# Performance work log

Measured on AMD Instinct MI355X. Metric: run time of the kernel, lower is better.

## Reference

```python
import math
import jax, jax.numpy as jnp
import numpy as np

RCR = 5.2   # radial cutoff
RCA = 3.5   # angular cutoff
B, N, T, KR, KA = 256, 24, 4, 16, 32

# static index tables (depend only on N)
_NIDX = np.array([[j for j in range(N) if j != i] for i in range(N)])  # [N, N-1] neighbors excluding self
_I1, _I2 = np.triu_indices(N - 1, k=1)                                  # pair combinations, P = C(N-1,2)


def setup_inputs() -> dict:
    key = jax.random.key(0)
    k1, k2 = jax.random.split(key)
    coords = jax.random.normal(k1, (B, N, 3), dtype=jnp.float32)
    atom_types = jax.random.randint(k2, (N,), 0, T)
    EtaR = jnp.full((T, KR), 16.0, dtype=jnp.float32)
    ShfR = jnp.tile(jnp.linspace(0.9, 4.95, KR, dtype=jnp.float32), (T, 1))
    Zeta = jnp.full((T, KA), 32.0, dtype=jnp.float32)
    ShfZ = jnp.tile(jnp.tile(jnp.linspace(0.9, 3.525, 8, dtype=jnp.float32), 4), (T, 1))
    EtaA = jnp.full((T, KA), 8.0, dtype=jnp.float32)
    ShfA = jnp.tile(jnp.repeat(jnp.linspace(0.3927, 2.7489, 4, dtype=jnp.float32), 8), (T, 1))
    return dict(coords=coords, atom_types=atom_types, EtaR=EtaR, ShfR=ShfR,
                Zeta=Zeta, ShfZ=ShfZ, EtaA=EtaA, ShfA=ShfA)


def reference(coords, atom_types, EtaR, ShfR, Zeta, ShfZ, EtaA, ShfA):
    # pairwise vectors excluding self: rij[b,i,k] = coords[b,i] - coords[b, j_k], j_k != i
    rij = coords[:, :, None, :] - coords[:, _NIDX, :]                      # [B,N,N-1,3]

    # gather per-atom parameter rows: [N, K] -> broadcast as [1,N,1,K]
    etaR = EtaR[atom_types][None, :, None, :]
    shfR = ShfR[atom_types][None, :, None, :]
    zeta = Zeta[atom_types][None, :, None, :]
    shfZ = ShfZ[atom_types][None, :, None, :]
    etaA = EtaA[atom_types][None, :, None, :]
    shfA = ShfA[atom_types][None, :, None, :]

    # ---- radial G2 ----
    dij = jnp.linalg.norm(rij, axis=3)                                     # [B,N,N-1]
    fij = 0.5 * (jnp.cos(dij * (math.pi / RCR)) + 1.0)
    g2 = jnp.sum(jnp.exp(-etaR * (dij[..., None] - shfR) ** 2) * fij[..., None], axis=2)  # [B,N,KR]

    # ---- angular G3 (ANI) ----
    r12 = rij[:, :, _I1]                                                   # [B,N,P,3]
    r13 = rij[:, :, _I2]
    d12 = jnp.linalg.norm(r12, axis=3)                                     # [B,N,P]
    d13 = jnp.linalg.norm(r13, axis=3)
    f12 = 0.5 * (jnp.cos(d12 * (math.pi / RCA)) + 1.0)
    f13 = 0.5 * (jnp.cos(d13 * (math.pi / RCA)) + 1.0)
    cosine = jnp.einsum('bnpc,bnpc->bnp', r12, r13) / (d12 * d13)
    cosine = jnp.clip(cosine, -1.0 + 1e-7, 1.0 - 1e-7)  # numerical guard for acos
    cosang = jnp.cos(jnp.arccos(cosine)[..., None] - shfA)                 # [B,N,P,KA]
    g3 = jnp.sum(
        2.0 ** (1.0 - zeta) * (1.0 + cosang) ** zeta
        * jnp.exp(-etaA * (0.5 * (d12 + d13)[..., None] - shfZ) ** 2)
        * (f12 * f13)[..., None],
        axis=2)                                                            # [B,N,KA]

    return jnp.concatenate((g2, g3), axis=2)                               # [B,N,KR+KA]
```

## Files before the change

### kernel.cpp

```cpp
#include <hip/hip_runtime.h>


constexpr int CB = 256;
constexpr int CN = 24;
constexpr int CKR = 16;
constexpr int CKA = 32;
constexpr int NN = 23;
constexpr int NP = 253;
constexpr int KOUT = CKR + CKA;
#define LOG2E 1.44269504088896340736f

__global__ __launch_bounds__(256) void ani_kernel(
    const float* __restrict__ coords, const int* __restrict__ atom_types,
    const float* __restrict__ EtaR, const float* __restrict__ ShfR,
    const float* __restrict__ Zeta, const float* __restrict__ ShfZ,
    const float* __restrict__ EtaA, const float* __restrict__ ShfA,
    float* __restrict__ out)
{
    __shared__ float s_rx[4][NN], s_ry[4][NN], s_rz[4][NN];
    __shared__ float s_d [4][NN], s_fA[4][NN], s_fR[4][NN];
    __shared__ unsigned char s_pa[NP], s_pb[NP];
    __shared__ float4 s_pair[4][NP + 1];

    const int wv   = threadIdx.x >> 6;
    const int lane = threadIdx.x & 63;
    const int row  = blockIdx.x * 4 + wv;
    const int b    = row / CN;
    const int i    = row - b * CN;

    for (int p = threadIdx.x; p < NP; p += 256) {
        int a = 0, pp = p;
        while (pp >= (NN - 1 - a)) { pp -= (NN - 1 - a); ++a; }
        s_pa[p] = (unsigned char)a;
        s_pb[p] = (unsigned char)(a + 1 + pp);
    }

    const float cix = coords[row*3+0], ciy = coords[row*3+1], ciz = coords[row*3+2];
    if (lane < NN) {
        const int j   = lane + (lane >= i ? 1 : 0);
        const int idx = (b * CN + j) * 3;
        const float dx = cix - coords[idx+0];
        const float dy = ciy - coords[idx+1];
        const float dz = ciz - coords[idx+2];
        const float d  = __builtin_amdgcn_sqrtf(dx*dx + dy*dy + dz*dz);
        s_rx[wv][lane] = dx; s_ry[wv][lane] = dy; s_rz[wv][lane] = dz;
        s_d [wv][lane] = d;
        s_fR[wv][lane] = 0.5f * (__cosf(d * (float)(3.14159265358979323846/5.2)) + 1.0f);
        s_fA[wv][lane] = 0.5f * (__cosf(d * (float)(3.14159265358979323846/3.5)) + 1.0f);
    }
    __syncthreads();

    #pragma unroll
    for (int it = 0; it < 4; ++it) {
        const int p = lane + it * 64;
        if (p < NP) {
            const int a = s_pa[p], c = s_pb[p];
            const float d12 = s_d[wv][a], d13 = s_d[wv][c];
            const float dot = s_rx[wv][a]*s_rx[wv][c]
                            + s_ry[wv][a]*s_ry[wv][c]
                            + s_rz[wv][a]*s_rz[wv][c];
            float cosv = dot * __builtin_amdgcn_rcpf(d12 * d13);
            cosv = fminf(fmaxf(cosv, -1.0f + 1e-7f), 1.0f - 1e-7f);
            const float sinv = __builtin_amdgcn_sqrtf(1.0f - cosv * cosv);
            const float avg  = 0.5f * (d12 + d13);
            const float ff2  = 2.0f * s_fA[wv][a] * s_fA[wv][c];
            s_pair[wv][p] = make_float4(cosv, sinv, avg, ff2);
        } else if (p == NP) {
            s_pair[wv][NP] = make_float4(0.0f, 0.0f, 0.0f, 0.0f);
        }
    }

    const int t = atom_types[i];

    {
        const int k = lane & 15, g = lane >> 4;
        const float eta = EtaR[t*CKR + k];
        const float shf = ShfR[t*CKR + k];
        float acc = 0.0f;
        for (int j = g; j < NN; j += 4) {
            const float x = s_d[wv][j] - shf;
            acc += __builtin_amdgcn_exp2f(-(eta * LOG2E) * x * x) * s_fR[wv][j];
        }
        acc += __shfl_xor(acc, 16, 64);
        acc += __shfl_xor(acc, 32, 64);
        if (lane < CKR) out[row * KOUT + k] = acc;
    }

    __syncthreads();

    {
        const int k = lane & 31, h = lane >> 5;
        const float zeta  = Zeta[t*CKA + k];
        const float shfZ  = ShfZ[t*CKA + k];
        const float etaAl = EtaA[t*CKA + k] * LOG2E;
        const float shfA  = ShfA[t*CKA + k];
        const float cA = __cosf(shfA), sA = __sinf(shfA);
        const float4* __restrict__ prow = &s_pair[wv][0];
        float acc = 0.0f;
        int p = h;
        #pragma unroll 4
        for (int it = 0; it < 127; ++it) {
            const float4 pd = prow[p]; p += 2;
            const float cosang = pd.x * cA + pd.y * sA;
            const float hh  = 0.5f * cosang + 0.5f;
            const float l2h = __log2f(hh);
            const float x   = pd.z - shfZ;
            const float e   = zeta * l2h - etaAl * x * x;
            acc += pd.w * __builtin_amdgcn_exp2f(e);
        }
        acc += __shfl_xor(acc, 32, 64);
        if (lane < CKA) out[row * KOUT + CKR + k] = acc;
    }
}

extern "C" void kernel_launch(void* const* d_in, const int* in_sizes, int n_in,
                              void* d_out, int out_size, void* d_ws, size_t ws_size,
                              hipStream_t stream) {
    const float* coords     = (const float*)d_in[0];
    const int*   atom_types = (const int*)  d_in[1];
    const float* EtaR       = (const float*)d_in[2];
    const float* ShfR       = (const float*)d_in[3];
    const float* Zeta       = (const float*)d_in[4];
    const float* ShfZ       = (const float*)d_in[5];
    const float* EtaA       = (const float*)d_in[6];
    const float* ShfA       = (const float*)d_in[7];
    float* out = (float*)d_out;

    dim3 grid((CB * CN) / 4), block(256);
    hipLaunchKernelGGL(ani_kernel, grid, block, 0, stream,
                       coords, atom_types, EtaR, ShfR, Zeta, ShfZ, EtaA, ShfA, out);
}
```

Before: 88.47 us.

## Factor angular terms into separable products with runtime-checked fast path

Adds a fast path for when the angular parameters have the separable structure (zeta of 32, one shared EtaA, ShfZ repeating with period 8, ShfA constant within blocks of 8). Each lane then takes its own pairs, computes 8 Gaussians and 4 power terms by repeated squaring, and accumulates all 32 outputs in registers. A butterfly shuffle reduction gathers the totals, and the old general loop stays as a fallback. This replaces 253 log2/exp2 evaluations per output with far fewer transcendentals, at the cost of more registers and a 32-wide shuffle reduction. It also swaps a per-pair reciprocal for precomputed per-neighbor reciprocals.

```diff
diff --git a/kernel.cpp b/kernel.cpp
--- a/kernel.cpp
+++ b/kernel.cpp
@@ -7,8 +7,21 @@
 constexpr int CKA = 32;
 constexpr int NN = 23;
 constexpr int NP = 253;
+constexpr int NPpad = 256;
 constexpr int KOUT = CKR + CKA;
 #define LOG2E 1.44269504088896340736f
+
+template<int MASK, int BIT, int HALF>
+__device__ inline void red_level(float* acc, int lane) {
+    const bool hi = (lane >> BIT) & 1;
+#pragma unroll
+    for (int j = 0; j < HALF; ++j) {
+        float send = hi ? acc[j] : acc[j + HALF];
+        float recv = __shfl_xor(send, MASK, 64);
+        float keep = hi ? acc[j + HALF] : acc[j];
+        acc[j] = keep + recv;
+    }
+}
 
 __global__ __launch_bounds__(256) void ani_kernel(
     const float* __restrict__ coords, const int* __restrict__ atom_types,
@@ -18,9 +31,9 @@
     float* __restrict__ out)
 {
     __shared__ float s_rx[4][NN], s_ry[4][NN], s_rz[4][NN];
-    __shared__ float s_d [4][NN], s_fA[4][NN], s_fR[4][NN];
+    __shared__ float s_d [4][NN], s_inv[4][NN], s_fA[4][NN], s_fR[4][NN];
     __shared__ unsigned char s_pa[NP], s_pb[NP];
-    __shared__ float4 s_pair[4][NP + 1];
+    __shared__ float4 s_pair[4][NPpad];
 
     const int wv   = threadIdx.x >> 6;
     const int lane = threadIdx.x & 63;
@@ -44,7 +57,8 @@
         const float dz = ciz - coords[idx+2];
         const float d  = __builtin_amdgcn_sqrtf(dx*dx + dy*dy + dz*dz);
         s_rx[wv][lane] = dx; s_ry[wv][lane] = dy; s_rz[wv][lane] = dz;
-        s_d [wv][lane] = d;
+        s_d  [wv][lane] = d;
+        s_inv[wv][lane] = __builtin_amdgcn_rcpf(d);
         s_fR[wv][lane] = 0.5f * (__cosf(d * (float)(3.14159265358979323846/5.2)) + 1.0f);
         s_fA[wv][lane] = 0.5f * (__cosf(d * (float)(3.14159265358979323846/3.5)) + 1.0f);
     }
@@ -59,14 +73,14 @@
             const float dot = s_rx[wv][a]*s_rx[wv][c]
                             + s_ry[wv][a]*s_ry[wv][c]
                             + s_rz[wv][a]*s_rz[wv][c];
-            float cosv = dot * __builtin_amdgcn_rcpf(d12 * d13);
+            float cosv = dot * (s_inv[wv][a] * s_inv[wv][c]);
             cosv = fminf(fmaxf(cosv, -1.0f + 1e-7f), 1.0f - 1e-7f);
             const float sinv = __builtin_amdgcn_sqrtf(1.0f - cosv * cosv);
             const float avg  = 0.5f * (d12 + d13);
             const float ff2  = 2.0f * s_fA[wv][a] * s_fA[wv][c];
             s_pair[wv][p] = make_float4(cosv, sinv, avg, ff2);
-        } else if (p == NP) {
-            s_pair[wv][NP] = make_float4(0.0f, 0.0f, 0.0f, 0.0f);
+        } else {
+            s_pair[wv][p] = make_float4(0.0f, 0.0f, 0.0f, 0.0f);
         }
     }
 
@@ -74,12 +88,12 @@
 
     {
         const int k = lane & 15, g = lane >> 4;
-        const float eta = EtaR[t*CKR + k];
+        const float eta = EtaR[t*CKR + k] * LOG2E;
         const float shf = ShfR[t*CKR + k];
         float acc = 0.0f;
         for (int j = g; j < NN; j += 4) {
             const float x = s_d[wv][j] - shf;
-            acc += __builtin_amdgcn_exp2f(-(eta * LOG2E) * x * x) * s_fR[wv][j];
+            acc += __builtin_amdgcn_exp2f(-eta * x * x) * s_fR[wv][j];
         }
         acc += __shfl_xor(acc, 16, 64);
         acc += __shfl_xor(acc, 32, 64);
@@ -88,12 +102,68 @@
 
     __syncthreads();
 
-    {
+    const float* __restrict__ Zt = ShfZ + t*CKA;
+    const float* __restrict__ At = ShfA + t*CKA;
+    const int kk = lane & 31;
+    const bool okl = (Zeta[t*CKA + kk] == 32.0f)
+                  && (EtaA[t*CKA + kk] == EtaA[t*CKA])
+                  && (Zt[kk] == Zt[kk & 7])
+                  && (At[kk] == At[kk & 24]);
+    const bool fast = __all(okl);
+
+    if (fast) {
+        const float cgau = -EtaA[t*CKA] * LOG2E;
+        float Zv[8], cAv[4], sAv[4];
+        #pragma unroll
+        for (int z = 0; z < 8; ++z) Zv[z] = Zt[z];
+        #pragma unroll
+        for (int a = 0; a < 4; ++a) {
+            const float sh = At[a * 8];
+            cAv[a] = __cosf(sh); sAv[a] = __sinf(sh);
+        }
+        float acc[32];
+        #pragma unroll
+        for (int k = 0; k < 32; ++k) acc[k] = 0.0f;
+
+        const float4* __restrict__ prow = &s_pair[wv][0];
+        #pragma unroll
+        for (int it = 0; it < 4; ++it) {
+            const float4 pd = prow[lane + it * 64];
+            float G[8];
+            #pragma unroll
+            for (int z = 0; z < 8; ++z) {
+                const float x = pd.z - Zv[z];
+                G[z] = __builtin_amdgcn_exp2f(cgau * x * x);
+            }
+            #pragma unroll
+            for (int a = 0; a < 4; ++a) {
+                const float cosang = pd.x * cAv[a] + pd.y * sAv[a];
+                const float hh  = 0.5f * cosang + 0.5f;
+                const float h2 = hh*hh, h4 = h2*h2, h8 = h4*h4, h16 = h8*h8;
+                const float Pa = (h16 * h16) * pd.w;
+                #pragma unroll
+                for (int z = 0; z < 8; ++z)
+                    acc[a*8 + z] = fmaf(Pa, G[z], acc[a*8 + z]);
+            }
+        }
+
+        red_level<1, 0, 16>(acc, lane);
+        red_level<2, 1,  8>(acc, lane);
+        red_level<4, 2,  4>(acc, lane);
+        red_level<8, 3,  2>(acc, lane);
+        red_level<16, 4, 1>(acc, lane);
+        acc[0] += __shfl_xor(acc[0], 32, 64);
+        if (lane < 32) {
+            const int k = ((lane & 1) << 4) | ((lane & 2) << 2) | (lane & 4)
+                        | ((lane & 8) >> 2) | ((lane & 16) >> 4);
+            out[row * KOUT + CKR + k] = acc[0];
+        }
+    } else {
         const int k = lane & 31, h = lane >> 5;
         const float zeta  = Zeta[t*CKA + k];
-        const float shfZ  = ShfZ[t*CKA + k];
+        const float shfZ  = Zt[k];
         const float etaAl = EtaA[t*CKA + k] * LOG2E;
-        const float shfA  = ShfA[t*CKA + k];
+        const float shfA  = At[k];
         const float cA = __cosf(shfA), sA = __sinf(shfA);
         const float4* __restrict__ prow = &s_pair[wv][0];
         float acc = 0.0f;
```

New measurement: 78.84 us. 1.12x faster.
